# Performance work log

Measured on AMD Instinct MI355X. Metric: run time of the kernel, lower is better.

Reference implementation:

```python
import jax, jax.numpy as jnp
import numpy as np

B, N, H = 8, 512, 256
HEADS, NLAYERS = 8, 3
NEG_SLOPE = 0.2
LN_EPS = 1e-5


def setup_inputs() -> dict:
    key = jax.random.key(0)
    ks = jax.random.split(key, 8)
    emb_inp = jax.random.normal(ks[0], (B, N, H), dtype=jnp.float32)
    rec_inp = jax.random.normal(ks[1], (B, N, 64), dtype=jnp.float32)
    mask = jax.random.randint(ks[2], (B, N, N), 0, 2, dtype=jnp.int32)
    dummy_arg = jnp.zeros((1,), dtype=jnp.float32)
    # GATConv params per layer: lin weight [H, heads*H], att_src/att_dst [heads, H], bias [H]
    W = jax.random.normal(ks[3], (NLAYERS, H, HEADS * H), dtype=jnp.float32) * 0.05
    att_src = jax.random.normal(ks[4], (NLAYERS, HEADS, H), dtype=jnp.float32) * 0.05
    att_dst = jax.random.normal(ks[5], (NLAYERS, HEADS, H), dtype=jnp.float32) * 0.05
    bias = jnp.zeros((NLAYERS, H), dtype=jnp.float32)
    ln_gamma = jnp.ones((H,), dtype=jnp.float32)
    ln_beta = jnp.zeros((H,), dtype=jnp.float32)
    return {"emb_inp": emb_inp, "rec_inp": rec_inp, "mask": mask,
            "dummy_arg": dummy_arg, "W": W, "att_src": att_src,
            "att_dst": att_dst, "bias": bias, "ln_gamma": ln_gamma,
            "ln_beta": ln_beta}


def reference(emb_inp, rec_inp, mask, dummy_arg, W, att_src, att_dst, bias, ln_gamma, ln_beta):
    # mask[b, i, j] != 0 means edge i -> j (PyG: source=row, target=col).
    # adj_t[b, j, i]: does target j receive from source i. GATConv adds self-loops.
    adj_t = jnp.swapaxes(mask, 1, 2).astype(bool) | jnp.eye(N, dtype=bool)[None]
    x = emb_inp
    for l in range(NLAYERS):
        Wl = W[l].reshape(H, HEADS, H)               # per-head projections
        xp = jnp.einsum('bni,ihk->bnhk', x, Wl)      # [B, N, heads, H]
        a_src = jnp.einsum('bnhk,hk->bnh', xp, att_src[l])
        a_dst = jnp.einsum('bnhk,hk->bnh', xp, att_dst[l])
        # logits[b, j(dst), i(src), h] = leaky_relu(a_src_i + a_dst_j)
        logits = jax.nn.leaky_relu(a_dst[:, :, None, :] + a_src[:, None, :, :], NEG_SLOPE)
        logits = jnp.where(adj_t[..., None], logits, -1e9)
        attn = jax.nn.softmax(logits, axis=2)        # softmax over sources per target
        out = jnp.einsum('bjih,bihk->bjhk', attn, xp).mean(axis=2) + bias[l]
        x = x + jax.nn.relu(out)                     # residual + ReLU per GAT layer
    y = emb_inp + jax.nn.relu(x)
    mu = y.mean(-1, keepdims=True)
    var = y.var(-1, keepdims=True)
    return (y - mu) / jnp.sqrt(var + LN_EPS) * ln_gamma + ln_beta
```

## Files before the change

kernel.cpp:

```cpp
#include <hip/hip_runtime.h>

#define BB 8
#define NN 512
#define HH 256
#define NHEADS 8

typedef __attribute__((ext_vector_type(8))) short bf16x8;
typedef __attribute__((ext_vector_type(4))) float f32x4;

__device__ __forceinline__ unsigned f2bf(float f) {
  unsigned u = __float_as_uint(f);
  u += 0x7fffu + ((u >> 16) & 1u);
  return u >> 16;
}
__device__ __forceinline__ float bf2f(unsigned short v) {
  return __uint_as_float(((unsigned)v) << 16);
}

__global__ __launch_bounds__(256) void prologue_kernel(const float* __restrict__ emb,
                                                       const int* __restrict__ mask,
                                                       const float* __restrict__ W,
                                                       float* __restrict__ x,
                                                       unsigned short* __restrict__ x_bf,
                                                       unsigned long long* __restrict__ adjT,
                                                       unsigned short* __restrict__ Wt,
                                                       float* __restrict__ asrcT,
                                                       float* __restrict__ adstT) {
  __shared__ float s[64][65];
  __shared__ unsigned short sadj[4][64];
  const int bid = blockIdx.x;
  const int t = threadIdx.x;
  if (bid < 1024) {
    const int b = bid & 7, chunk = bid >> 3;
    const size_t i4 = ((size_t)b * 128 + chunk) * 256 + t;
    const float4 v = ((const float4*)emb)[i4];
    ((float4*)x)[i4] = v;
    uint2 p;
    p.x = f2bf(v.x) | (f2bf(v.y) << 16);
    p.y = f2bf(v.z) | (f2bf(v.w) << 16);
    ((uint2*)x_bf)[i4] = p;
  } else if (bid < 1536) {
    const int bb = bid - 1024;
    const int b = bb & 7, w = (bb >> 3) & 7, jc = bb >> 6;
    const int jloc = t & 63, qq = t >> 6;
    const int j = jc * 64 + jloc;
    unsigned short bits = 0;
#pragma unroll
    for (int qi = 0; qi < 16; ++qi) {
      const int q = qq * 16 + qi;
      const int i = w * 64 + q;
      const int m = mask[((size_t)b * NN + i) * NN + j];
      if (m != 0 || i == j) bits |= (unsigned short)(1u << qi);
    }
    sadj[qq][jloc] = bits;
    __syncthreads();
    if (t < 64) {
      const unsigned long long word = (unsigned long long)sadj[0][t] |
                                      ((unsigned long long)sadj[1][t] << 16) |
                                      ((unsigned long long)sadj[2][t] << 32) |
                                      ((unsigned long long)sadj[3][t] << 48);
      adjT[((size_t)b * NN + jc * 64 + t) * 8 + w] = word;
    }
  } else if (bid < 1920) {
    const int wb = bid - 1536;
    const int l = wb >> 7;
    const int r = wb & 127;
    const int mt = r & 31, ct = r >> 5;
    const int hk0 = mt * 64, c0 = ct * 64;
    const int tr = t >> 6, tc = t & 63;
#pragma unroll
    for (int p = 0; p < 16; ++p) {
      const int row = p * 4 + tr;
      s[row][tc] = W[(size_t)l * 524288 + (size_t)(c0 + row) * 2048 + hk0 + tc];
    }
    __syncthreads();
#pragma unroll
    for (int p = 0; p < 16; ++p) {
      const int hkl = p * 4 + tr;
      Wt[(size_t)l * 524288 + (size_t)(hk0 + hkl) * 256 + c0 + tc] =
          (unsigned short)f2bf(s[tc][hkl]);
    }
  } else {
    const int i4 = (bid - 1920) * 256 + t;
    const float4 z = {0.f, 0.f, 0.f, 0.f};
    if (i4 < 8192) ((float4*)asrcT)[i4] = z;
    else           ((float4*)adstT)[i4 - 8192] = z;
  }
}

__global__ __launch_bounds__(256, 2) void proj_mfma_kernel(const unsigned short* __restrict__ Wt_l,
                                                           const unsigned short* __restrict__ x_bf,
                                                           const float* __restrict__ att_src_l,
                                                           const float* __restrict__ att_dst_l,
                                                           unsigned short* __restrict__ xpTT,
                                                           float* __restrict__ asrcT,
                                                           float* __restrict__ adstT) {
  __shared__ __align__(16) unsigned char lds[32768];
  const int t = threadIdx.x;
  const int lane = t & 63, wave = t >> 6;
  const int wj = wave >> 1, wk = wave & 1;

  const int bid = blockIdx.x;
  const int b = bid & 7;
  const int r = bid >> 3;
  const int mt = r & 15, nt = r >> 4;
  const int hk0 = mt * 128, n0 = nt * 128;

  const int tr = t >> 1, th = t & 1;
  const size_t aBase = (size_t)(hk0 + tr) * 256 + th * 16;
  const size_t bBase = ((size_t)(b * NN + n0 + tr)) * 256 + th * 16;
  const unsigned sw_w = ((tr >> 1) & 3) << 4;
  const unsigned w0 = tr * 64 + ((th * 32 + 0) ^ sw_w);
  const unsigned w1 = tr * 64 + ((th * 32 + 16) ^ sw_w);

  uint4 ra0, ra1, rb0, rb1;
  {
    ra0 = *(const uint4*)(Wt_l + aBase);
    ra1 = *(const uint4*)(Wt_l + aBase + 8);
    rb0 = *(const uint4*)(x_bf + bBase);
    rb1 = *(const uint4*)(x_bf + bBase + 8);
  }

  const f32x4 z4 = {0.f, 0.f, 0.f, 0.f};
  f32x4 acc[4][4];
#pragma unroll
  for (int fr = 0; fr < 4; ++fr)
#pragma unroll
    for (int fc = 0; fc < 4; ++fc) acc[fr][fc] = z4;

  for (int s = 0; s < 8; ++s) {
    const unsigned boff = (s & 1) << 14;
    *(uint4*)(lds + boff + w0) = ra0;
    *(uint4*)(lds + boff + w1) = ra1;
    *(uint4*)(lds + boff + 8192 + w0) = rb0;
    *(uint4*)(lds + boff + 8192 + w1) = rb1;
    __syncthreads();
    if (s < 7) {
      const size_t off = (size_t)(s + 1) * 32;
      ra0 = *(const uint4*)(Wt_l + aBase + off);
      ra1 = *(const uint4*)(Wt_l + aBase + off + 8);
      rb0 = *(const uint4*)(x_bf + bBase + off);
      rb1 = *(const uint4*)(x_bf + bBase + off + 8);
    }
    bf16x8 af[4], bfr[4];
#pragma unroll
    for (int fr = 0; fr < 4; ++fr) {
      const int rA = wj * 64 + fr * 16 + (lane & 15);
      af[fr] = *(const bf16x8*)(lds + boff + rA * 64 +
                                (((lane >> 4) * 16) ^ (((rA >> 1) & 3) << 4)));
    }
#pragma unroll
    for (int fc = 0; fc < 4; ++fc) {
      const int rB = wk * 64 + fc * 16 + (lane & 15);
      bfr[fc] = *(const bf16x8*)(lds + boff + 8192 + rB * 64 +
                                 (((lane >> 4) * 16) ^ (((rB >> 1) & 3) << 4)));
    }
#pragma unroll
    for (int fr = 0; fr < 4; ++fr)
#pragma unroll
      for (int fc = 0; fc < 4; ++fc)
        acc[fr][fc] = __builtin_amdgcn_mfma_f32_16x16x32_bf16(af[fr], bfr[fc], acc[fr][fc], 0, 0, 0);
  }

  unsigned short* xpb = xpTT + (size_t)b * 2048 * NN;
#pragma unroll
  for (int fr = 0; fr < 4; ++fr) {
    const int row0 = hk0 + wj * 64 + fr * 16 + (lane >> 4) * 4;
#pragma unroll
    for (int fc = 0; fc < 4; ++fc) {
      const int col = n0 + wk * 64 + fc * 16 + (lane & 15);
#pragma unroll
      for (int rr = 0; rr < 4; ++rr)
        xpb[(size_t)(row0 + rr) * NN + col] = (unsigned short)f2bf(acc[fr][fc][rr]);
    }
  }

  float wsv[4][4], wdv[4][4];
#pragma unroll
  for (int fr = 0; fr < 4; ++fr) {
    const int row0 = hk0 + wj * 64 + fr * 16 + (lane >> 4) * 4;
#pragma unroll
    for (int rr = 0; rr < 4; ++rr) {
      wsv[fr][rr] = att_src_l[row0 + rr];
      wdv[fr][rr] = att_dst_l[row0 + rr];
    }
  }
  const int bh = b * 8 + (mt >> 1);
#pragma unroll
  for (int fc = 0; fc < 4; ++fc) {
    float as = 0.f, ad = 0.f;
#pragma unroll
    for (int fr = 0; fr < 4; ++fr)
#pragma unroll
      for (int rr = 0; rr < 4; ++rr) {
        as = fmaf(acc[fr][fc][rr], wsv[fr][rr], as);
        ad = fmaf(acc[fr][fc][rr], wdv[fr][rr], ad);
      }
    as += __shfl_xor(as, 16);
    as += __shfl_xor(as, 32);
    ad += __shfl_xor(ad, 16);
    ad += __shfl_xor(ad, 32);
    if ((lane >> 4) == 0) {
      const int col = n0 + wk * 64 + fc * 16 + lane;
      atomicAdd(&asrcT[(size_t)bh * NN + col], as);
      atomicAdd(&adstT[(size_t)bh * NN + col], ad);
    }
  }
}

__global__ __launch_bounds__(256, 2) void agg_fused_kernel(const unsigned short* __restrict__ xpTT,
                                                           const float* __restrict__ asrcT,
                                                           const float* __restrict__ adstT,
                                                           const unsigned long long* __restrict__ adjT,
                                                           float* __restrict__ out_part) {
  __shared__ __align__(16) unsigned char lds[40960];
  __shared__ float s_as[NN];
  __shared__ __align__(16) unsigned char s_adjw[4096];
  __shared__ float s_dinv[64];
  const int t = threadIdx.x;
  const int lane = t & 63, wave = t >> 6;
  const int wk = wave;

  const int bid = blockIdx.x;
  const int b = bid & 7;
  const int r = bid >> 3;
  const int jt = r & 7, hs = r >> 3;
  const int j0 = jt * 64;
  const int bh = b * 8 + hs;

  const int tr4 = t >> 2, th4 = t & 3;
  const int tr2 = t >> 1, th2 = t & 1;

  s_as[t] = asrcT[(size_t)bh * NN + t];
  s_as[t + 256] = asrcT[(size_t)bh * NN + t + 256];
  *(uint4*)(s_adjw + tr4 * 64 + th4 * 16) =
      *(const uint4*)((const unsigned char*)adjT + ((size_t)(b * NN + j0 + tr4)) * 64 + th4 * 16);
  const float adv = adstT[(size_t)bh * NN + j0 + tr4];
  __syncthreads();

  const unsigned sw4 = ((tr4 >> 1) & 3) << 4;
  const unsigned wA = tr4 * 64 + ((th4 * 16) ^ sw4);
  const unsigned sw2 = ((tr2 >> 1) & 3) << 4;
  const unsigned wB0 = tr2 * 64 + ((th2 * 32 + 0) ^ sw2);
  const unsigned wB1 = tr2 * 64 + ((th2 * 32 + 16) ^ sw2);
  const size_t bBase0 = ((size_t)bh * HH + tr2) * NN + th2 * 16;
  const size_t bBase1 = ((size_t)bh * HH + tr2 + 128) * NN + th2 * 16;

  float esum = 0.f;
  uint4 pe, rb0, rb1, rb2, rb3;
  auto GENP = [&](int s, uint4& o) {
    const unsigned bits = s_adjw[tr4 * 64 + s * 4 + th4];
    const float* ap = s_as + s * 32 + th4 * 8;
    unsigned wds[4];
#pragma unroll
    for (int p = 0; p < 4; ++p) {
      float z0 = adv + ap[2 * p];
      float z1 = adv + ap[2 * p + 1];
      z0 = fmaxf(z0, 0.2f * z0);
      z1 = fmaxf(z1, 0.2f * z1);
      float e0 = __expf(z0);
      float e1 = __expf(z1);
      e0 = ((bits >> (2 * p)) & 1u) ? e0 : 0.f;
      e1 = ((bits >> (2 * p + 1)) & 1u) ? e1 : 0.f;
      esum += e0 + e1;
      wds[p] = f2bf(e0) | (f2bf(e1) << 16);
    }
    o.x = wds[0]; o.y = wds[1]; o.z = wds[2]; o.w = wds[3];
  };
  auto BLOAD = [&](int s, uint4& r0, uint4& r1, uint4& r2, uint4& r3) {
    r0 = *(const uint4*)(xpTT + bBase0 + s * 32);
    r1 = *(const uint4*)(xpTT + bBase0 + s * 32 + 8);
    r2 = *(const uint4*)(xpTT + bBase1 + s * 32);
    r3 = *(const uint4*)(xpTT + bBase1 + s * 32 + 8);
  };

  GENP(0, pe);
  BLOAD(0, rb0, rb1, rb2, rb3);

  const f32x4 z4 = {0.f, 0.f, 0.f, 0.f};
  f32x4 acc[4][4];
#pragma unroll
  for (int fr = 0; fr < 4; ++fr)
#pragma unroll
    for (int fc = 0; fc < 4; ++fc) acc[fr][fc] = z4;

  for (int s = 0; s < 16; ++s) {
    const unsigned boff = (s & 1) ? 20480u : 0u;
    *(uint4*)(lds + boff + wA) = pe;
    *(uint4*)(lds + boff + 4096 + wB0) = rb0;
    *(uint4*)(lds + boff + 4096 + wB1) = rb1;
    *(uint4*)(lds + boff + 4096 + wB0 + 8192) = rb2;
    *(uint4*)(lds + boff + 4096 + wB1 + 8192) = rb3;
    __syncthreads();
    if (s < 15) {
      BLOAD(s + 1, rb0, rb1, rb2, rb3);
      GENP(s + 1, pe);
    }
    bf16x8 af[4], bfr[4];
#pragma unroll
    for (int fr = 0; fr < 4; ++fr) {
      const int rA = fr * 16 + (lane & 15);
      af[fr] = *(const bf16x8*)(lds + boff + rA * 64 +
                                (((lane >> 4) * 16) ^ (((rA >> 1) & 3) << 4)));
    }
#pragma unroll
    for (int fc = 0; fc < 4; ++fc) {
      const int rB = wk * 64 + fc * 16 + (lane & 15);
      bfr[fc] = *(const bf16x8*)(lds + boff + 4096 + rB * 64 +
                                 (((lane >> 4) * 16) ^ (((rB >> 1) & 3) << 4)));
    }
#pragma unroll
    for (int fr = 0; fr < 4; ++fr)
#pragma unroll
      for (int fc = 0; fc < 4; ++fc)
        acc[fr][fc] = __builtin_amdgcn_mfma_f32_16x16x32_bf16(af[fr], bfr[fc], acc[fr][fc], 0, 0, 0);
  }

  esum += __shfl_xor(esum, 1);
  esum += __shfl_xor(esum, 2);
  __syncthreads();
  if (th4 == 0) s_dinv[tr4] = 1.f / (8.f * esum);
  __syncthreads();

  float* op = out_part + ((size_t)hs * BB + b) * NN * HH;
#pragma unroll
  for (int fr = 0; fr < 4; ++fr) {
    const int jl0 = fr * 16 + (lane >> 4) * 4;
#pragma unroll
    for (int fc = 0; fc < 4; ++fc) {
      const int kcol = wk * 64 + fc * 16 + (lane & 15);
#pragma unroll
      for (int rr = 0; rr < 4; ++rr)
        op[(size_t)(j0 + jl0 + rr) * HH + kcol] = acc[fr][fc][rr] * s_dinv[jl0 + rr];
    }
  }
}

__global__ __launch_bounds__(256) void out_epi_kernel(const float* __restrict__ out_part,
                                                      const float* __restrict__ bias_l,
                                                      float* __restrict__ x,
                                                      unsigned short* __restrict__ x_bf,
                                                      float* __restrict__ asrcT,
                                                      float* __restrict__ adstT) {
  const int bid = blockIdx.x;
  const int t = threadIdx.x;
  if (bid < 64) {
    const int i4 = bid * 256 + t;
    const float4 z = {0.f, 0.f, 0.f, 0.f};
    if (i4 < 8192) ((float4*)asrcT)[i4] = z;
    else           ((float4*)adstT)[i4 - 8192] = z;
  }
  const int b = bid & 7, nn = bid >> 3;
  const size_t idx = ((size_t)(b * NN + nn)) * HH + t;
  const size_t S = (size_t)BB * NN * HH;
  float o = bias_l[t];
#pragma unroll
  for (int s = 0; s < 8; ++s) o += out_part[s * S + idx];
  const float xn = x[idx] + fmaxf(o, 0.f);
  x[idx] = xn;
  x_bf[idx] = (unsigned short)f2bf(xn);
}

__global__ __launch_bounds__(256) void epi_ln_kernel(const float* __restrict__ out_part,
                                                     const float* __restrict__ bias_l,
                                                     const float* __restrict__ x,
                                                     const float* __restrict__ emb,
                                                     const float* __restrict__ gamma,
                                                     const float* __restrict__ beta,
                                                     float* __restrict__ out) {
  const int bid = blockIdx.x;
  const int t = threadIdx.x;
  const int b = bid & 7, nn = bid >> 3;
  const size_t idx = ((size_t)(b * NN + nn)) * HH + t;
  const size_t S = (size_t)BB * NN * HH;
  float o = bias_l[t];
#pragma unroll
  for (int s = 0; s < 8; ++s) o += out_part[s * S + idx];
  const float xn = x[idx] + fmaxf(o, 0.f);
  const float y = emb[idx] + fmaxf(xn, 0.f);
  float s1 = y, s2 = y * y;
#pragma unroll
  for (int off = 32; off > 0; off >>= 1) {
    s1 += __shfl_down(s1, off);
    s2 += __shfl_down(s2, off);
  }
  __shared__ float rs[4], rs2[4], stat[2];
  const int wave = t >> 6, lane = t & 63;
  if (lane == 0) { rs[wave] = s1; rs2[wave] = s2; }
  __syncthreads();
  if (t == 0) {
    const float S1 = rs[0] + rs[1] + rs[2] + rs[3];
    const float S2 = rs2[0] + rs2[1] + rs2[2] + rs2[3];
    const float mu = S1 * (1.f / 256.f);
    const float var = S2 * (1.f / 256.f) - mu * mu;
    stat[0] = mu;
    stat[1] = rsqrtf(var + 1e-5f);
  }
  __syncthreads();
  out[idx] = (y - stat[0]) * stat[1] * gamma[t] + beta[t];
}

extern "C" void kernel_launch(void* const* d_in, const int* in_sizes, int n_in,
                              void* d_out, int out_size, void* d_ws, size_t ws_size,
                              hipStream_t stream) {
  const float* emb    = (const float*)d_in[0];
  const int*   mask   = (const int*)d_in[2];
  const float* W      = (const float*)d_in[4];
  const float* aw_src = (const float*)d_in[5];
  const float* aw_dst = (const float*)d_in[6];
  const float* bias   = (const float*)d_in[7];
  const float* gamma  = (const float*)d_in[8];
  const float* beta   = (const float*)d_in[9];
  float* out = (float*)d_out;

  char* ws = (char*)d_ws;
  unsigned short* xpTT = (unsigned short*)(ws);
  float* out_part      = (float*)(ws + 16777216);
  float* x             = (float*)(ws + 50331648);
  unsigned short* x_bf = (unsigned short*)(ws + 54525952);
  float* asrcT         = (float*)(ws + 56623104);
  float* adstT         = (float*)(ws + 56754176);
  unsigned long long* adjT = (unsigned long long*)(ws + 57016320);
  unsigned short* Wt   = (unsigned short*)(ws + 57278464);

  prologue_kernel<<<1984, 256, 0, stream>>>(emb, mask, W, x, x_bf, adjT, Wt, asrcT, adstT);

  for (int l = 0; l < 3; ++l) {
    proj_mfma_kernel<<<512, 256, 0, stream>>>(Wt + (size_t)l * 524288, x_bf,
                                              aw_src + l * NHEADS * HH, aw_dst + l * NHEADS * HH,
                                              xpTT, asrcT, adstT);
    agg_fused_kernel<<<512, 256, 0, stream>>>(xpTT, asrcT, adstT, adjT, out_part);
    if (l < 2)
      out_epi_kernel<<<BB * NN, 256, 0, stream>>>(out_part, bias + l * HH, x, x_bf, asrcT, adstT);
  }
  epi_ln_kernel<<<BB * NN, 256, 0, stream>>>(out_part, bias + 2 * HH, x, emb, gamma, beta, out);
}
```

Measured before the change: 128.7 us.

## Load MFMA B operands directly from global memory, bypassing LDS staging

In the projection kernel, both MFMA operand fragments are now loaded straight from global memory into registers with a register double buffer, and LDS plus block barriers are removed entirely. In the aggregation kernel, the xp operand is loaded per wave directly into fragment registers while only the generated attention tile still goes through a smaller LDS ping-pong buffer. The aim is to cut LDS write/read traffic, barriers and LDS footprint, which could raise occupancy. The cost is less coalesced global loads (16-byte strided rows per lane) and higher register pressure from the doubled fragment arrays.

```diff
diff --git a/kernel.cpp b/kernel.cpp
--- a/kernel.cpp
+++ b/kernel.cpp
@@ -95,7 +95,6 @@
                                                            unsigned short* __restrict__ xpTT,
                                                            float* __restrict__ asrcT,
                                                            float* __restrict__ adstT) {
-  __shared__ __align__(16) unsigned char lds[32768];
   const int t = threadIdx.x;
   const int lane = t & 63, wave = t >> 6;
   const int wj = wave >> 1, wk = wave & 1;
@@ -106,19 +105,15 @@
   const int mt = r & 15, nt = r >> 4;
   const int hk0 = mt * 128, n0 = nt * 128;
 
-  const int tr = t >> 1, th = t & 1;
-  const size_t aBase = (size_t)(hk0 + tr) * 256 + th * 16;
-  const size_t bBase = ((size_t)(b * NN + n0 + tr)) * 256 + th * 16;
-  const unsigned sw_w = ((tr >> 1) & 3) << 4;
-  const unsigned w0 = tr * 64 + ((th * 32 + 0) ^ sw_w);
-  const unsigned w1 = tr * 64 + ((th * 32 + 16) ^ sw_w);
-
-  uint4 ra0, ra1, rb0, rb1;
-  {
-    ra0 = *(const uint4*)(Wt_l + aBase);
-    ra1 = *(const uint4*)(Wt_l + aBase + 8);
-    rb0 = *(const uint4*)(x_bf + bBase);
-    rb1 = *(const uint4*)(x_bf + bBase + 8);
+  const int lr = lane & 15, lo = lane >> 4;
+  const unsigned short* ap0 = Wt_l + (size_t)(hk0 + wj * 64 + lr) * 256 + lo * 8;
+  const unsigned short* bp0 = x_bf + ((size_t)(b * NN + n0 + wk * 64 + lr)) * 256 + lo * 8;
+
+  bf16x8 af[2][4], bfv[2][4];
+#pragma unroll
+  for (int q = 0; q < 4; ++q) {
+    af[0][q]  = *(const bf16x8*)(ap0 + q * 4096);
+    bfv[0][q] = *(const bf16x8*)(bp0 + q * 4096);
   }
 
   const f32x4 z4 = {0.f, 0.f, 0.f, 0.f};
@@ -128,38 +123,22 @@
 #pragma unroll
     for (int fc = 0; fc < 4; ++fc) acc[fr][fc] = z4;
 
+#pragma unroll
   for (int s = 0; s < 8; ++s) {
-    const unsigned boff = (s & 1) << 14;
-    *(uint4*)(lds + boff + w0) = ra0;
-    *(uint4*)(lds + boff + w1) = ra1;
-    *(uint4*)(lds + boff + 8192 + w0) = rb0;
-    *(uint4*)(lds + boff + 8192 + w1) = rb1;
-    __syncthreads();
+    const int cur = s & 1, nxt = cur ^ 1;
     if (s < 7) {
-      const size_t off = (size_t)(s + 1) * 32;
-      ra0 = *(const uint4*)(Wt_l + aBase + off);
-      ra1 = *(const uint4*)(Wt_l + aBase + off + 8);
-      rb0 = *(const uint4*)(x_bf + bBase + off);
-      rb1 = *(const uint4*)(x_bf + bBase + off + 8);
-    }
-    bf16x8 af[4], bfr[4];
-#pragma unroll
-    for (int fr = 0; fr < 4; ++fr) {
-      const int rA = wj * 64 + fr * 16 + (lane & 15);
-      af[fr] = *(const bf16x8*)(lds + boff + rA * 64 +
-                                (((lane >> 4) * 16) ^ (((rA >> 1) & 3) << 4)));
-    }
-#pragma unroll
-    for (int fc = 0; fc < 4; ++fc) {
-      const int rB = wk * 64 + fc * 16 + (lane & 15);
-      bfr[fc] = *(const bf16x8*)(lds + boff + 8192 + rB * 64 +
-                                 (((lane >> 4) * 16) ^ (((rB >> 1) & 3) << 4)));
+#pragma unroll
+      for (int q = 0; q < 4; ++q) {
+        af[nxt][q]  = *(const bf16x8*)(ap0 + q * 4096 + (s + 1) * 32);
+        bfv[nxt][q] = *(const bf16x8*)(bp0 + q * 4096 + (s + 1) * 32);
+      }
     }
 #pragma unroll
     for (int fr = 0; fr < 4; ++fr)
 #pragma unroll
       for (int fc = 0; fc < 4; ++fc)
-        acc[fr][fc] = __builtin_amdgcn_mfma_f32_16x16x32_bf16(af[fr], bfr[fc], acc[fr][fc], 0, 0, 0);
+        acc[fr][fc] = __builtin_amdgcn_mfma_f32_16x16x32_bf16(af[cur][fr], bfv[cur][fc],
+                                                              acc[fr][fc], 0, 0, 0);
   }
 
   unsigned short* xpb = xpTT + (size_t)b * 2048 * NN;
@@ -213,7 +192,7 @@
                                                            const float* __restrict__ adstT,
                                                            const unsigned long long* __restrict__ adjT,
                                                            float* __restrict__ out_part) {
-  __shared__ __align__(16) unsigned char lds[40960];
+  __shared__ __align__(16) unsigned char ldsA[8192];
   __shared__ float s_as[NN];
   __shared__ __align__(16) unsigned char s_adjw[4096];
   __shared__ float s_dinv[64];
@@ -229,7 +208,7 @@
   const int bh = b * 8 + hs;
 
   const int tr4 = t >> 2, th4 = t & 3;
-  const int tr2 = t >> 1, th2 = t & 1;
+  const int lr = lane & 15, lo = lane >> 4;
 
   s_as[t] = asrcT[(size_t)bh * NN + t];
   s_as[t + 256] = asrcT[(size_t)bh * NN + t + 256];
@@ -240,14 +219,10 @@
 
   const unsigned sw4 = ((tr4 >> 1) & 3) << 4;
   const unsigned wA = tr4 * 64 + ((th4 * 16) ^ sw4);
-  const unsigned sw2 = ((tr2 >> 1) & 3) << 4;
-  const unsigned wB0 = tr2 * 64 + ((th2 * 32 + 0) ^ sw2);
-  const unsigned wB1 = tr2 * 64 + ((th2 * 32 + 16) ^ sw2);
-  const size_t bBase0 = ((size_t)bh * HH + tr2) * NN + th2 * 16;
-  const size_t bBase1 = ((size_t)bh * HH + tr2 + 128) * NN + th2 * 16;
+  const unsigned short* bp0 = xpTT + ((size_t)bh * HH + wk * 64 + lr) * NN + lo * 8;
 
   float esum = 0.f;
-  uint4 pe, rb0, rb1, rb2, rb3;
+  uint4 pe;
   auto GENP = [&](int s, uint4& o) {
     const unsigned bits = s_adjw[tr4 * 64 + s * 4 + th4];
     const float* ap = s_as + s * 32 + th4 * 8;
@@ -267,15 +242,11 @@
     }
     o.x = wds[0]; o.y = wds[1]; o.z = wds[2]; o.w = wds[3];
   };
-  auto BLOAD = [&](int s, uint4& r0, uint4& r1, uint4& r2, uint4& r3) {
-    r0 = *(const uint4*)(xpTT + bBase0 + s * 32);
-    r1 = *(const uint4*)(xpTT + bBase0 + s * 32 + 8);
-    r2 = *(const uint4*)(xpTT + bBase1 + s * 32);
-    r3 = *(const uint4*)(xpTT + bBase1 + s * 32 + 8);
-  };
 
   GENP(0, pe);
-  BLOAD(0, rb0, rb1, rb2, rb3);
+  bf16x8 fbA[4], fbB[4];
+#pragma unroll
+  for (int q = 0; q < 4; ++q) fbA[q] = *(const bf16x8*)(bp0 + q * 8192);
 
   const f32x4 z4 = {0.f, 0.f, 0.f, 0.f};
   f32x4 acc[4][4];
@@ -284,36 +255,46 @@
 #pragma unroll
     for (int fc = 0; fc < 4; ++fc) acc[fr][fc] = z4;
 
-  for (int s = 0; s < 16; ++s) {
-    const unsigned boff = (s & 1) ? 20480u : 0u;
-    *(uint4*)(lds + boff + wA) = pe;
-    *(uint4*)(lds + boff + 4096 + wB0) = rb0;
-    *(uint4*)(lds + boff + 4096 + wB1) = rb1;
-    *(uint4*)(lds + boff + 4096 + wB0 + 8192) = rb2;
-    *(uint4*)(lds + boff + 4096 + wB1 + 8192) = rb3;
+  bf16x8 af[4];
+#pragma unroll 1
+  for (int ss = 0; ss < 8; ++ss) {
+    *(uint4*)(ldsA + wA) = pe;
     __syncthreads();
-    if (s < 15) {
-      BLOAD(s + 1, rb0, rb1, rb2, rb3);
-      GENP(s + 1, pe);
-    }
-    bf16x8 af[4], bfr[4];
+    {
+      GENP(2 * ss + 1, pe);
+#pragma unroll
+      for (int q = 0; q < 4; ++q)
+        fbB[q] = *(const bf16x8*)(bp0 + q * 8192 + (2 * ss + 1) * 32);
+    }
 #pragma unroll
     for (int fr = 0; fr < 4; ++fr) {
-      const int rA = fr * 16 + (lane & 15);
-      af[fr] = *(const bf16x8*)(lds + boff + rA * 64 +
-                                (((lane >> 4) * 16) ^ (((rA >> 1) & 3) << 4)));
-    }
-#pragma unroll
-    for (int fc = 0; fc < 4; ++fc) {
-      const int rB = wk * 64 + fc * 16 + (lane & 15);
-      bfr[fc] = *(const bf16x8*)(lds + boff + 4096 + rB * 64 +
-                                 (((lane >> 4) * 16) ^ (((rB >> 1) & 3) << 4)));
+      const int rA = fr * 16 + lr;
+      af[fr] = *(const bf16x8*)(ldsA + rA * 64 + ((lo * 16) ^ (((rA >> 1) & 3) << 4)));
     }
 #pragma unroll
     for (int fr = 0; fr < 4; ++fr)
 #pragma unroll
       for (int fc = 0; fc < 4; ++fc)
-        acc[fr][fc] = __builtin_amdgcn_mfma_f32_16x16x32_bf16(af[fr], bfr[fc], acc[fr][fc], 0, 0, 0);
+        acc[fr][fc] = __builtin_amdgcn_mfma_f32_16x16x32_bf16(af[fr], fbA[fc], acc[fr][fc], 0, 0, 0);
+
+    *(uint4*)(ldsA + 4096 + wA) = pe;
+    __syncthreads();
+    if (ss < 7) {
+      GENP(2 * ss + 2, pe);
+#pragma unroll
+      for (int q = 0; q < 4; ++q)
+        fbA[q] = *(const bf16x8*)(bp0 + q * 8192 + (2 * ss + 2) * 32);
+    }
+#pragma unroll
+    for (int fr = 0; fr < 4; ++fr) {
+      const int rA = fr * 16 + lr;
+      af[fr] = *(const bf16x8*)(ldsA + 4096 + rA * 64 + ((lo * 16) ^ (((rA >> 1) & 3) << 4)));
+    }
+#pragma unroll
+    for (int fr = 0; fr < 4; ++fr)
+#pragma unroll
+      for (int fc = 0; fc < 4; ++fc)
+        acc[fr][fc] = __builtin_amdgcn_mfma_f32_16x16x32_bf16(af[fr], fbB[fc], acc[fr][fc], 0, 0, 0);
   }
 
   esum += __shfl_xor(esum, 1);
```

Result: slower. 162.9 us (+26.6%).
